# Optimization experiments

Measured on AMD Instinct MI355X. Metric: run time of the kernel, lower is better.

Reference implementation:

```python
import jax, jax.numpy as jnp
import numpy as np

B, T, C, H = 4, 2048, 1024, 16


def setup_inputs() -> dict:
    key = jax.random.key(0)
    k1, k2, k3 = jax.random.split(key, 3)
    x = jax.random.normal(k1, (B, T, C), dtype=jnp.float32)
    Wqkv = jax.random.normal(k2, (C, 3 * C), dtype=jnp.float32) * 0.02
    bqkv = jnp.zeros((3 * C,), dtype=jnp.float32)
    Wproj = jax.random.normal(k3, (C, C), dtype=jnp.float32) * 0.02
    bproj = jnp.zeros((C,), dtype=jnp.float32)
    return {"x": x, "Wqkv": Wqkv, "bqkv": bqkv, "Wproj": Wproj, "bproj": bproj}


def reference(x, Wqkv, bqkv, Wproj, bproj):
    Bx, Tx, Cx = x.shape
    head = Cx // H
    qkv = x @ Wqkv + bqkv                      # [B,T,3C]
    q, k, v = jnp.split(qkv, 3, axis=-1)
    q = q.reshape(Bx, Tx, H, head)
    k = k.reshape(Bx, Tx, H, head)
    v = v.reshape(Bx, Tx, H, head)
    scale = 1.0 / jnp.sqrt(jnp.asarray(head, dtype=x.dtype))
    scores = jnp.einsum('bqhd,bkhd->bhqk', q, k) * scale   # [B,H,T,T]
    causal = jnp.tril(jnp.ones((Tx, Tx), dtype=bool))       # [T,T]
    neg = jnp.finfo(x.dtype).min
    scores = jnp.where(causal[None, None, :, :], scores, neg)
    probs = jax.nn.softmax(scores, axis=-1)
    y = jnp.einsum('bhqk,bkhd->bqhd', probs, v).reshape(Bx, Tx, Cx)
    return y @ Wproj + bproj
```

## Files before the change

### kernel.cpp

```cpp
#include <hip/hip_runtime.h>
#include <stdint.h>

#define BB 4
#define TT 2048
#define CC 1024
#define HH 16

typedef __bf16 bf16x8 __attribute__((ext_vector_type(8)));
typedef float f32x4 __attribute__((ext_vector_type(4)));
typedef float f32x16 __attribute__((ext_vector_type(16)));
typedef unsigned short ushort8 __attribute__((ext_vector_type(8)));
typedef unsigned short ushort4v __attribute__((ext_vector_type(4)));

__device__ __forceinline__ unsigned short f2b(float f) {
    union { float f; unsigned u; } v; v.f = f;
    unsigned r = v.u + 0x7FFFu + ((v.u >> 16) & 1u);
    return (unsigned short)(r >> 16);
}
__device__ __forceinline__ unsigned pack2(float a, float b) {
    union { float f; unsigned u; } ua, ub; ua.f = a; ub.f = b;
    return __builtin_amdgcn_perm(ub.u + 0x8000u, ua.u + 0x8000u, 0x07060302u);
}
__device__ __forceinline__ float fexp2(float x) {
#if __has_builtin(__builtin_amdgcn_exp2f)
    return __builtin_amdgcn_exp2f(x);
#else
    return exp2f(x);
#endif
}
#define LOG2E 1.4426950408889634f

#define ASYNC16(gp, lp) __builtin_amdgcn_global_load_lds( \
    (const __attribute__((address_space(1))) void*)(gp),  \
    (__attribute__((address_space(3))) void*)(lp), 16, 0, 0)

__global__ __launch_bounds__(256) void k_cast(const float* __restrict__ in,
                                              unsigned short* __restrict__ out, int n) {
    int i = (blockIdx.x * 256 + threadIdx.x) * 4;
    if (i >= n) return;
    float4 v = *(const float4*)(in + i);
    ushort4v o;
    o.x = f2b(v.x); o.y = f2b(v.y); o.z = f2b(v.z); o.w = f2b(v.w);
    *(ushort4v*)(out + i) = o;
}

__global__ __launch_bounds__(256) void k_transpose_bf16(const float* __restrict__ in,
                                                        unsigned short* __restrict__ out,
                                                        int R, int Cc) {
    __shared__ float tile[32][33];
    int bx = blockIdx.x * 32, by = blockIdx.y * 32;
    int tx = threadIdx.x, ty = threadIdx.y;
    for (int i = 0; i < 32; i += 8)
        tile[ty + i][tx] = in[(size_t)(by + ty + i) * Cc + bx + tx];
    __syncthreads();
    for (int i = 0; i < 32; i += 8)
        out[(size_t)(bx + ty + i) * R + by + tx] = f2b(tile[tx][ty + i]);
}

#define QSCALE 0.125f

__global__ __launch_bounds__(256, 2) void k_gemmqkv(const unsigned short* __restrict__ A,
                                                    const unsigned short* __restrict__ Bt,
                                                    const float* __restrict__ bias,
                                                    unsigned short* __restrict__ qo,
                                                    unsigned short* __restrict__ ko,
                                                    unsigned short* __restrict__ vo,
                                                    int M, int N, int K) {
    __shared__ unsigned short sm[3 * 12288];
    const int t = threadIdx.x;
    const int lane = t & 63;
    const int c = lane & 15, qd = lane >> 4;
    const int wave = t >> 6;
    const int wr = wave >> 1, wc = wave & 1;
    const int bm = blockIdx.x * 256, bn = blockIdx.y * 128;

    f32x4 acc[8][4] = {};

    const int srow = t >> 2;
    const int sch = (t & 3) ^ ((t >> 3) & 3);
    const unsigned short* Ap = A + (size_t)(bm + srow) * K + sch * 8;
    const unsigned short* Bp = Bt + (size_t)(bn + srow) * K + sch * 8;
    const int fch = qd ^ ((c >> 1) & 3);
    const int NT = K >> 5;

#define STG_P0(buf, tt_) do {                                              \
        const unsigned short* ga_ = Ap + (size_t)(tt_) * 32;               \
        const unsigned short* gb_ = Bp + (size_t)(tt_) * 32;               \
        ASYNC16(ga_,                  &sm[(buf) * 12288 + t * 8]);         \
        ASYNC16(ga_ + (size_t)64 * K, &sm[(buf) * 12288 + 2048 + t * 8]);  \
        ASYNC16(gb_,                  &sm[(buf) * 12288 + 8192 + t * 8]);  \
    } while (0)
#define STG_P1(buf, tt_) do {                                              \
        const unsigned short* ga_ = Ap + (size_t)(tt_) * 32;               \
        const unsigned short* gb_ = Bp + (size_t)(tt_) * 32;               \
        ASYNC16(ga_ + (size_t)128 * K, &sm[(buf) * 12288 + 4096 + t * 8]); \
        ASYNC16(ga_ + (size_t)192 * K, &sm[(buf) * 12288 + 6144 + t * 8]); \
        ASYNC16(gb_ + (size_t)64 * K,  &sm[(buf) * 12288 + 10240 + t * 8]);\
    } while (0)

    STG_P0(0, 0); STG_P1(0, 0);
    STG_P0(1, 1); STG_P1(1, 1);
    asm volatile("s_waitcnt vmcnt(6)" ::: "memory");
    __builtin_amdgcn_s_barrier();

    int bc = 0, b1 = 1, bs = 2;
    for (int tt = 0; tt < NT; ++tt) {
        const unsigned short* Ab = &sm[bc * 12288];
        const unsigned short* Bb = &sm[bc * 12288 + 8192];
        bf16x8 bf_[4], af[4];

        if (tt + 2 < NT) STG_P0(bs, tt + 2);
#pragma unroll
        for (int j = 0; j < 4; j++)
            bf_[j] = *(const bf16x8*)&Bb[(wc * 64 + j * 16 + c) * 32 + fch * 8];
#pragma unroll
        for (int i = 0; i < 4; i++)
            af[i] = *(const bf16x8*)&Ab[(wr * 128 + i * 16 + c) * 32 + fch * 8];
        __builtin_amdgcn_s_barrier();
        asm volatile("s_waitcnt lgkmcnt(0)" ::: "memory");
        __builtin_amdgcn_sched_barrier(0);
        __builtin_amdgcn_s_setprio(1);
#pragma unroll
        for (int i = 0; i < 4; i++)
#pragma unroll
            for (int j = 0; j < 4; j++)
                acc[i][j] = __builtin_amdgcn_mfma_f32_16x16x32_bf16(af[i], bf_[j], acc[i][j], 0, 0, 0);
        __builtin_amdgcn_s_setprio(0);
        __builtin_amdgcn_s_barrier();

        if (tt + 2 < NT) STG_P1(bs, tt + 2);
#pragma unroll
        for (int i = 0; i < 4; i++)
            af[i] = *(const bf16x8*)&Ab[(wr * 128 + 64 + i * 16 + c) * 32 + fch * 8];
        if (tt + 2 < NT) {
            asm volatile("s_waitcnt vmcnt(6)" ::: "memory");
        } else if (tt + 1 < NT) {
            asm volatile("s_waitcnt vmcnt(0)" ::: "memory");
        }
        __builtin_amdgcn_s_barrier();
        asm volatile("s_waitcnt lgkmcnt(0)" ::: "memory");
        __builtin_amdgcn_sched_barrier(0);
        __builtin_amdgcn_s_setprio(1);
#pragma unroll
        for (int i = 0; i < 4; i++)
#pragma unroll
            for (int j = 0; j < 4; j++)
                acc[i + 4][j] = __builtin_amdgcn_mfma_f32_16x16x32_bf16(af[i], bf_[j], acc[i + 4][j], 0, 0, 0);
        __builtin_amdgcn_s_setprio(0);
        __builtin_amdgcn_s_barrier();

        int tmp = bc; bc = b1; b1 = bs; bs = tmp;
    }
#undef STG_P0
#undef STG_P1

#pragma unroll
    for (int j = 0; j < 4; j++) {
        float bv = bias[bn + wc * 64 + j * 16 + c];
#pragma unroll
        for (int i = 0; i < 8; i++)
#pragma unroll
            for (int r = 0; r < 4; r++)
                acc[i][j][r] += bv;
    }

    if (bn < 2048) {
        unsigned short* dst = (bn < 1024) ? qo : ko;
        const int dcol0 = (bn < 1024) ? bn : bn - 1024;
        const float sc = (bn < 1024) ? QSCALE : 1.0f;
        __syncthreads();
#pragma unroll
        for (int i = 0; i < 8; i++) {
            int lr0 = wr * 128 + i * 16 + qd * 4;
#pragma unroll
            for (int j = 0; j < 4; j++) {
                int col = wc * 64 + j * 16 + c;
#pragma unroll
                for (int r = 0; r < 4; r++)
                    sm[(lr0 + r) * 136 + col] = f2b(acc[i][j][r] * sc);
            }
        }
        __syncthreads();
#pragma unroll
        for (int op = 0; op < 16; op++) {
            int cid = op * 256 + t;
            int lr = cid >> 4;
            int ch = (cid & 15) * 8;
            ushort8 v = *(ushort8*)&sm[lr * 136 + ch];
            *(ushort8*)&dst[(size_t)(bm + lr) * 1024 + dcol0 + ch] = v;
        }
    } else {
        const int bseg = bm >> 11;
        const int bmt = bm & 2047;
        __syncthreads();
#pragma unroll
        for (int i = 0; i < 8; i++) {
            int tok = wr * 128 + i * 16 + qd * 4;
#pragma unroll
            for (int j = 0; j < 4; j++) {
                int dl = wc * 64 + j * 16 + c;
                ushort4v pk;
                pk.x = f2b(acc[i][j][0]); pk.y = f2b(acc[i][j][1]);
                pk.z = f2b(acc[i][j][2]); pk.w = f2b(acc[i][j][3]);
                *(ushort4v*)&sm[dl * 264 + tok] = pk;
            }
        }
        __syncthreads();
#pragma unroll
        for (int op = 0; op < 16; op++) {
            int cid = op * 256 + t;
            int dl = cid >> 5;
            int ch = (cid & 31) * 8;
            ushort8 v = *(ushort8*)&sm[dl * 264 + ch];
            int d = (bn - 2048) + dl;
            *(ushort8*)&vo[((size_t)bseg * 1024 + d) * 2048 + bmt + ch] = v;
        }
    }
}

template <int MODE>
__global__ __launch_bounds__(256) void k_gemm(const unsigned short* __restrict__ A,
                                              const unsigned short* __restrict__ Bt,
                                              const float* __restrict__ bias,
                                              float* __restrict__ outf,
                                              unsigned short* __restrict__ qo,
                                              unsigned short* __restrict__ ko,
                                              unsigned short* __restrict__ vo,
                                              int M, int N, int K) {
    __shared__ unsigned short sm[8704];
    unsigned short* As = sm;
    unsigned short* Bs = sm + 4096;
    const int t = threadIdx.x;
    const int lane = t & 63;
    const int c = lane & 15, qd = lane >> 4;
    const int wave = t >> 6;
    const int wr = (wave >> 1) * 64, wc = (wave & 1) * 64;
    const int bm = blockIdx.x * 128, bn = blockIdx.y * 128;

    f32x4 acc[4][4] = {};

    const unsigned short* Ap = A + (size_t)(bm + (t >> 2)) * K + (t & 3) * 8;
    const unsigned short* Bp = Bt + (size_t)(bn + (t >> 2)) * K + (t & 3) * 8;
    unsigned short* Asw = &As[t * 8];
    unsigned short* Bsw = &Bs[t * 8];

    for (int k0 = 0; k0 < K; k0 += 32) {
        __syncthreads();
        ASYNC16(Ap + k0, Asw);
        ASYNC16(Ap + (size_t)64 * K + k0, Asw + 2048);
        ASYNC16(Bp + k0, Bsw);
        ASYNC16(Bp + (size_t)64 * K + k0, Bsw + 2048);
        __syncthreads();
        bf16x8 af[4], bfr[4];
        for (int i = 0; i < 4; i++)
            af[i] = *(const bf16x8*)&As[(wr + i * 16 + c) * 32 + qd * 8];
        for (int j = 0; j < 4; j++)
            bfr[j] = *(const bf16x8*)&Bs[(wc + j * 16 + c) * 32 + qd * 8];
        for (int i = 0; i < 4; i++)
            for (int j = 0; j < 4; j++)
                acc[i][j] = __builtin_amdgcn_mfma_f32_16x16x32_bf16(af[i], bfr[j], acc[i][j], 0, 0, 0);
    }

    for (int j = 0; j < 4; j++) {
        float bv = bias[bn + wc + j * 16 + c];
        for (int i = 0; i < 4; i++)
            for (int r = 0; r < 4; r++)
                acc[i][j][r] += bv;
    }

    if (MODE == 0) {
        float* smf = (float*)sm;
        for (int p = 0; p < 4; p++) {
            __syncthreads();
            int lr0 = (wr >> 2) + qd * 4;
            for (int j = 0; j < 4; j++) {
                int col = wc + j * 16 + c;
                for (int r = 0; r < 4; r++)
                    smf[(lr0 + r) * 132 + col] = acc[p][j][r];
            }
            __syncthreads();
            for (int op = 0; op < 4; op++) {
                int lr = (t >> 5) + op * 8;
                int ch = (t & 31) * 4;
                float4 v = *(float4*)&smf[lr * 132 + ch];
                int grow = bm + (lr >> 4) * 64 + 16 * p + (lr & 15);
                *(float4*)&outf[(size_t)grow * N + bn + ch] = v;
            }
        }
    }
}

__global__ __launch_bounds__(256, 4) void k_attn(const unsigned short* __restrict__ q16,
                                                 const unsigned short* __restrict__ k16,
                                                 const unsigned short* __restrict__ vT16,
                                                 unsigned short* __restrict__ y16) {
    const int h = blockIdx.y, b = blockIdx.z;
    const int qi = (((int)blockIdx.x + h) & 15) ^ ((b & 1) ? 15 : 0);
    __shared__ unsigned short smem[128 * 72];
    unsigned short* q_s = smem;
    unsigned short* k_s = smem;
    unsigned short* vt_s = smem + 64 * 72;
    const int t = threadIdx.x, lane = t & 63, wave = t >> 6;
    const int l31 = lane & 31, hl = lane >> 5;
    const int wq = wave * 32;

    {
        int row = t >> 1, c32 = (t & 1) * 32;
        const unsigned short* src = q16 + ((size_t)(b * TT + qi * 128 + row)) * CC + h * 64 + c32;
        ushort8 v0 = *(const ushort8*)(src);
        ushort8 v1 = *(const ushort8*)(src + 8);
        ushort8 v2 = *(const ushort8*)(src + 16);
        ushort8 v3 = *(const ushort8*)(src + 24);
        *(ushort8*)&q_s[row * 72 + c32] = v0;
        *(ushort8*)&q_s[row * 72 + c32 + 8] = v1;
        *(ushort8*)&q_s[row * 72 + c32 + 16] = v2;
        *(ushort8*)&q_s[row * 72 + c32 + 24] = v3;
    }
    __syncthreads();
    bf16x8 qf[4];
    for (int s = 0; s < 4; s++)
        qf[s] = *(const bf16x8*)&q_s[(wq + l31) * 72 + s * 16 + hl * 8];

    f32x16 oacc[2] = {};
    float m = -3e38f, l = 0.f;
    const int qmaxw = qi * 128 + wq + 31;
    const int qminw = qi * 128 + wq;
    const int qg = qi * 128 + wq + l31;
    const int jn = 2 * qi + 2;
    const unsigned short* kbase = k16 + (size_t)b * TT * CC + h * 64;
    const unsigned short* vbase = vT16 + (((size_t)b * 16 + h) * 64) * TT;

    const int row = t >> 2, c16 = (t & 3) * 16;
    const unsigned short* ksrc = kbase + (size_t)row * CC + c16;
    const unsigned short* vsrc = vbase + (size_t)row * TT + c16;
    ushort8 ka = *(const ushort8*)ksrc, kb = *(const ushort8*)(ksrc + 8);
    ushort8 va = *(const ushort8*)vsrc, vb = *(const ushort8*)(vsrc + 8);

    for (int j = 0; j < jn; j++) {
        __syncthreads();
        *(ushort8*)&k_s[row * 72 + c16] = ka;
        *(ushort8*)&k_s[row * 72 + c16 + 8] = kb;
        *(ushort8*)&vt_s[row * 72 + c16] = va;
        *(ushort8*)&vt_s[row * 72 + c16 + 8] = vb;
        __syncthreads();
        if (j + 1 < jn) {
            const unsigned short* kn = ksrc + (size_t)(j + 1) * 64 * CC;
            const unsigned short* vn = vsrc + (j + 1) * 64;
            ka = *(const ushort8*)kn; kb = *(const ushort8*)(kn + 8);
            va = *(const ushort8*)vn; vb = *(const ushort8*)(vn + 8);
        }
        if (j * 64 > qmaxw) continue;

        f32x16 sacc[2] = {};
        for (int c2 = 0; c2 < 2; c2++)
            for (int s = 0; s < 4; s++) {
                bf16x8 kf = *(const bf16x8*)&k_s[(c2 * 32 + l31) * 72 + s * 16 + hl * 8];
                sacc[c2] = __builtin_amdgcn_mfma_f32_32x32x16_bf16(kf, qf[s], sacc[c2], 0, 0, 0);
            }

        if (j * 64 + 63 > qminw) {
            for (int c2 = 0; c2 < 2; c2++)
                for (int r = 0; r < 16; r++) {
                    int kvg = j * 64 + c2 * 32 + (r & 3) + 8 * (r >> 2) + 4 * hl;
                    if (kvg > qg) sacc[c2][r] = -1e30f;
                }
        }

        float mx = -1e30f;
        for (int c2 = 0; c2 < 2; c2++)
            for (int r = 0; r < 16; r++) mx = fmaxf(mx, sacc[c2][r]);
        mx = fmaxf(mx, __shfl_xor(mx, 32, 64));
        float mn = fmaxf(m, mx);
        float negmnl = -mn * LOG2E;
        float alpha = fexp2(fmaf(m, LOG2E, negmnl));
        m = mn;
        float sum = 0.f;
        unsigned pg[2][4][2];
        for (int c2 = 0; c2 < 2; c2++)
            for (int g = 0; g < 4; g++) {
                float p0 = fexp2(fmaf(sacc[c2][g * 4 + 0], LOG2E, negmnl));
                float p1 = fexp2(fmaf(sacc[c2][g * 4 + 1], LOG2E, negmnl));
                float p2 = fexp2(fmaf(sacc[c2][g * 4 + 2], LOG2E, negmnl));
                float p3 = fexp2(fmaf(sacc[c2][g * 4 + 3], LOG2E, negmnl));
                sum += (p0 + p1) + (p2 + p3);
                pg[c2][g][0] = pack2(p0, p1);
                pg[c2][g][1] = pack2(p2, p3);
            }
        sum += __shfl_xor(sum, 32, 64);
        l = l * alpha + sum;
        if (__ballot(alpha != 1.0f)) {
            for (int c2 = 0; c2 < 2; c2++)
                for (int r = 0; r < 16; r++) oacc[c2][r] *= alpha;
        }

        bf16x8 pf[4];
        for (int c2 = 0; c2 < 2; c2++)
            for (int pr = 0; pr < 2; pr++) {
                unsigned se0 = hl ? pg[c2][2 * pr][0] : pg[c2][2 * pr + 1][0];
                unsigned se1 = hl ? pg[c2][2 * pr][1] : pg[c2][2 * pr + 1][1];
                unsigned r0 = (unsigned)__shfl_xor((int)se0, 32, 64);
                unsigned r1 = (unsigned)__shfl_xor((int)se1, 32, 64);
                union { unsigned u[4]; bf16x8 v; } fr;
                fr.u[0] = hl ? r0 : pg[c2][2 * pr][0];
                fr.u[1] = hl ? r1 : pg[c2][2 * pr][1];
                fr.u[2] = hl ? pg[c2][2 * pr + 1][0] : r0;
                fr.u[3] = hl ? pg[c2][2 * pr + 1][1] : r1;
                pf[c2 * 2 + pr] = fr.v;
            }

        for (int s = 0; s < 4; s++)
            for (int c2o = 0; c2o < 2; c2o++) {
                bf16x8 vf = *(const bf16x8*)&vt_s[(c2o * 32 + l31) * 72 + s * 16 + hl * 8];
                oacc[c2o] = __builtin_amdgcn_mfma_f32_32x32x16_bf16(vf, pf[s], oacc[c2o], 0, 0, 0);
            }
    }

    float rl = 1.0f / l;
    size_t rowb = ((size_t)b * TT + qg) * CC + h * 64;
    for (int c2 = 0; c2 < 2; c2++)
        for (int g = 0; g < 4; g++) {
            ushort4v pk;
            pk.x = f2b(oacc[c2][g * 4 + 0] * rl);
            pk.y = f2b(oacc[c2][g * 4 + 1] * rl);
            pk.z = f2b(oacc[c2][g * 4 + 2] * rl);
            pk.w = f2b(oacc[c2][g * 4 + 3] * rl);
            *(ushort4v*)&y16[rowb + c2 * 32 + g * 8 + hl * 4] = pk;
        }
}

extern "C" void kernel_launch(void* const* d_in, const int* in_sizes, int n_in,
                              void* d_out, int out_size, void* d_ws, size_t ws_size,
                              hipStream_t stream) {
    const float* x     = (const float*)d_in[0];
    const float* Wqkv  = (const float*)d_in[1];
    const float* bqkv  = (const float*)d_in[2];
    const float* Wproj = (const float*)d_in[3];
    const float* bproj = (const float*)d_in[4];
    float* out = (float*)d_out;

    const int M = BB * TT;
    unsigned short* x16    = (unsigned short*)d_ws;
    unsigned short* y16    = x16;
    unsigned short* wqkvT  = x16 + (size_t)M * CC;
    unsigned short* wprojT = wqkvT + (size_t)3 * CC * CC;
    unsigned short* q16    = wprojT + (size_t)CC * CC;
    unsigned short* k16    = q16 + (size_t)M * CC;
    unsigned short* vT16   = k16 + (size_t)M * CC;

    k_cast<<<(M * CC) / 1024, 256, 0, stream>>>(x, x16, M * CC);
    k_transpose_bf16<<<dim3(3 * CC / 32, CC / 32), dim3(32, 8), 0, stream>>>(Wqkv, wqkvT, CC, 3 * CC);
    k_transpose_bf16<<<dim3(CC / 32, CC / 32), dim3(32, 8), 0, stream>>>(Wproj, wprojT, CC, CC);
    k_gemmqkv<<<dim3(M / 256, 3 * CC / 128), 256, 0, stream>>>(x16, wqkvT, bqkv,
                                                               q16, k16, vT16, M, 3 * CC, CC);
    k_attn<<<dim3(TT / 128, HH, BB), 256, 0, stream>>>(q16, k16, vT16, y16);
    k_gemm<0><<<dim3(M / 128, CC / 128), 256, 0, stream>>>(y16, wprojT, bproj, out,
                                                           nullptr, nullptr, nullptr, M, CC, CC);
}
```

Baseline: 257.7 us.

## Pair causal query tiles per block, lazy rescale, permlane swap, MFMA priority

```diff
diff --git a/kernel.cpp b/kernel.cpp
--- a/kernel.cpp
+++ b/kernel.cpp
@@ -295,7 +295,6 @@
                                                  const unsigned short* __restrict__ vT16,
                                                  unsigned short* __restrict__ y16) {
     const int h = blockIdx.y, b = blockIdx.z;
-    const int qi = (((int)blockIdx.x + h) & 15) ^ ((b & 1) ? 15 : 0);
     __shared__ unsigned short smem[128 * 72];
     unsigned short* q_s = smem;
     unsigned short* k_s = smem;
@@ -303,129 +302,138 @@
     const int t = threadIdx.x, lane = t & 63, wave = t >> 6;
     const int l31 = lane & 31, hl = lane >> 5;
     const int wq = wave * 32;
-
-    {
-        int row = t >> 1, c32 = (t & 1) * 32;
-        const unsigned short* src = q16 + ((size_t)(b * TT + qi * 128 + row)) * CC + h * 64 + c32;
-        ushort8 v0 = *(const ushort8*)(src);
-        ushort8 v1 = *(const ushort8*)(src + 8);
-        ushort8 v2 = *(const ushort8*)(src + 16);
-        ushort8 v3 = *(const ushort8*)(src + 24);
-        *(ushort8*)&q_s[row * 72 + c32] = v0;
-        *(ushort8*)&q_s[row * 72 + c32 + 8] = v1;
-        *(ushort8*)&q_s[row * 72 + c32 + 16] = v2;
-        *(ushort8*)&q_s[row * 72 + c32 + 24] = v3;
-    }
-    __syncthreads();
-    bf16x8 qf[4];
-    for (int s = 0; s < 4; s++)
-        qf[s] = *(const bf16x8*)&q_s[(wq + l31) * 72 + s * 16 + hl * 8];
-
-    f32x16 oacc[2] = {};
-    float m = -3e38f, l = 0.f;
-    const int qmaxw = qi * 128 + wq + 31;
-    const int qminw = qi * 128 + wq;
-    const int qg = qi * 128 + wq + l31;
-    const int jn = 2 * qi + 2;
     const unsigned short* kbase = k16 + (size_t)b * TT * CC + h * 64;
     const unsigned short* vbase = vT16 + (((size_t)b * 16 + h) * 64) * TT;
-
     const int row = t >> 2, c16 = (t & 3) * 16;
     const unsigned short* ksrc = kbase + (size_t)row * CC + c16;
     const unsigned short* vsrc = vbase + (size_t)row * TT + c16;
-    ushort8 ka = *(const ushort8*)ksrc, kb = *(const ushort8*)(ksrc + 8);
-    ushort8 va = *(const ushort8*)vsrc, vb = *(const ushort8*)(vsrc + 8);
-
-    for (int j = 0; j < jn; j++) {
-        __syncthreads();
-        *(ushort8*)&k_s[row * 72 + c16] = ka;
-        *(ushort8*)&k_s[row * 72 + c16 + 8] = kb;
-        *(ushort8*)&vt_s[row * 72 + c16] = va;
-        *(ushort8*)&vt_s[row * 72 + c16 + 8] = vb;
-        __syncthreads();
-        if (j + 1 < jn) {
-            const unsigned short* kn = ksrc + (size_t)(j + 1) * 64 * CC;
-            const unsigned short* vn = vsrc + (j + 1) * 64;
-            ka = *(const ushort8*)kn; kb = *(const ushort8*)(kn + 8);
-            va = *(const ushort8*)vn; vb = *(const ushort8*)(vn + 8);
-        }
-        if (j * 64 > qmaxw) continue;
-
-        f32x16 sacc[2] = {};
-        for (int c2 = 0; c2 < 2; c2++)
-            for (int s = 0; s < 4; s++) {
-                bf16x8 kf = *(const bf16x8*)&k_s[(c2 * 32 + l31) * 72 + s * 16 + hl * 8];
-                sacc[c2] = __builtin_amdgcn_mfma_f32_32x32x16_bf16(kf, qf[s], sacc[c2], 0, 0, 0);
-            }
-
-        if (j * 64 + 63 > qminw) {
+
+    for (int half = 0; half < 2; half++) {
+        const int qi = half ? 15 - (int)blockIdx.x : (int)blockIdx.x;
+
+        __syncthreads();
+        {
+            int qrow = t >> 1, c32 = (t & 1) * 32;
+            const unsigned short* src = q16 + ((size_t)(b * TT + qi * 128 + qrow)) * CC + h * 64 + c32;
+            ushort8 v0 = *(const ushort8*)(src);
+            ushort8 v1 = *(const ushort8*)(src + 8);
+            ushort8 v2 = *(const ushort8*)(src + 16);
+            ushort8 v3 = *(const ushort8*)(src + 24);
+            *(ushort8*)&q_s[qrow * 72 + c32] = v0;
+            *(ushort8*)&q_s[qrow * 72 + c32 + 8] = v1;
+            *(ushort8*)&q_s[qrow * 72 + c32 + 16] = v2;
+            *(ushort8*)&q_s[qrow * 72 + c32 + 24] = v3;
+        }
+        __syncthreads();
+        bf16x8 qf[4];
+        for (int s = 0; s < 4; s++)
+            qf[s] = *(const bf16x8*)&q_s[(wq + l31) * 72 + s * 16 + hl * 8];
+
+        f32x16 oacc[2] = {};
+        float m = -3e38f, l = 0.f;
+        const int qmaxw = qi * 128 + wq + 31;
+        const int qminw = qi * 128 + wq;
+        const int qg = qi * 128 + wq + l31;
+        const int jn = 2 * qi + 2;
+
+        ushort8 ka = *(const ushort8*)ksrc, kb = *(const ushort8*)(ksrc + 8);
+        ushort8 va = *(const ushort8*)vsrc, vb = *(const ushort8*)(vsrc + 8);
+
+        for (int j = 0; j < jn; j++) {
+            __syncthreads();
+            *(ushort8*)&k_s[row * 72 + c16] = ka;
+            *(ushort8*)&k_s[row * 72 + c16 + 8] = kb;
+            *(ushort8*)&vt_s[row * 72 + c16] = va;
+            *(ushort8*)&vt_s[row * 72 + c16 + 8] = vb;
+            __syncthreads();
+            if (j + 1 < jn) {
+                const unsigned short* kn = ksrc + (size_t)(j + 1) * 64 * CC;
+                const unsigned short* vn = vsrc + (j + 1) * 64;
+                ka = *(const ushort8*)kn; kb = *(const ushort8*)(kn + 8);
+                va = *(const ushort8*)vn; vb = *(const ushort8*)(vn + 8);
+            }
+            if (j * 64 > qmaxw) continue;
+
+            f32x16 sacc[2] = {};
+            __builtin_amdgcn_s_setprio(1);
             for (int c2 = 0; c2 < 2; c2++)
-                for (int r = 0; r < 16; r++) {
-                    int kvg = j * 64 + c2 * 32 + (r & 3) + 8 * (r >> 2) + 4 * hl;
-                    if (kvg > qg) sacc[c2][r] = -1e30f;
+                for (int s = 0; s < 4; s++) {
+                    bf16x8 kf = *(const bf16x8*)&k_s[(c2 * 32 + l31) * 72 + s * 16 + hl * 8];
+                    sacc[c2] = __builtin_amdgcn_mfma_f32_32x32x16_bf16(kf, qf[s], sacc[c2], 0, 0, 0);
                 }
-        }
-
-        float mx = -1e30f;
-        for (int c2 = 0; c2 < 2; c2++)
-            for (int r = 0; r < 16; r++) mx = fmaxf(mx, sacc[c2][r]);
-        mx = fmaxf(mx, __shfl_xor(mx, 32, 64));
-        float mn = fmaxf(m, mx);
-        float negmnl = -mn * LOG2E;
-        float alpha = fexp2(fmaf(m, LOG2E, negmnl));
-        m = mn;
-        float sum = 0.f;
-        unsigned pg[2][4][2];
+            __builtin_amdgcn_s_setprio(0);
+
+            if (j * 64 + 63 > qminw) {
+                for (int c2 = 0; c2 < 2; c2++)
+                    for (int r = 0; r < 16; r++) {
+                        int kvg = j * 64 + c2 * 32 + (r & 3) + 8 * (r >> 2) + 4 * hl;
+                        if (kvg > qg) sacc[c2][r] = -1e30f;
+                    }
+            }
+
+            float mx = -1e30f;
+            for (int c2 = 0; c2 < 2; c2++)
+                for (int r = 0; r < 16; r += 2)
+                    mx = fmaxf(mx, fmaxf(sacc[c2][r], sacc[c2][r + 1]));
+            mx = fmaxf(mx, __shfl_xor(mx, 32, 64));
+            if (!__all(mx <= m + 8.0f)) {
+                float mn = fmaxf(m, mx);
+                float negl = -mn * LOG2E;
+                float alpha = fexp2(fmaf(m, LOG2E, negl));
+                m = mn;
+                l *= alpha;
+                for (int c2 = 0; c2 < 2; c2++)
+                    for (int r = 0; r < 16; r++) oacc[c2][r] *= alpha;
+            }
+            float negmnl = -m * LOG2E;
+            float sum = 0.f;
+            unsigned pg[2][4][2];
+            for (int c2 = 0; c2 < 2; c2++)
+                for (int g = 0; g < 4; g++) {
+                    float p0 = fexp2(fmaf(sacc[c2][g * 4 + 0], LOG2E, negmnl));
+                    float p1 = fexp2(fmaf(sacc[c2][g * 4 + 1], LOG2E, negmnl));
+                    float p2 = fexp2(fmaf(sacc[c2][g * 4 + 2], LOG2E, negmnl));
+                    float p3 = fexp2(fmaf(sacc[c2][g * 4 + 3], LOG2E, negmnl));
+                    sum += (p0 + p1) + (p2 + p3);
+                    pg[c2][g][0] = pack2(p0, p1);
+                    pg[c2][g][1] = pack2(p2, p3);
+                }
+            sum += __shfl_xor(sum, 32, 64);
+            l += sum;
+
+            bf16x8 pf[4];
+            for (int c2 = 0; c2 < 2; c2++)
+                for (int pr = 0; pr < 2; pr++) {
+                    unsigned a0 = pg[c2][2 * pr][0], b0 = pg[c2][2 * pr + 1][0];
+                    unsigned a1 = pg[c2][2 * pr][1], b1 = pg[c2][2 * pr + 1][1];
+                    asm("v_permlane32_swap_b32 %0, %1" : "+v"(a0), "+v"(b0));
+                    asm("v_permlane32_swap_b32 %0, %1" : "+v"(a1), "+v"(b1));
+                    union { unsigned u[4]; bf16x8 v; } fr;
+                    fr.u[0] = a0; fr.u[1] = a1; fr.u[2] = b0; fr.u[3] = b1;
+                    pf[c2 * 2 + pr] = fr.v;
+                }
+
+            __builtin_amdgcn_s_setprio(1);
+            for (int s = 0; s < 4; s++)
+                for (int c2o = 0; c2o < 2; c2o++) {
+                    bf16x8 vf = *(const bf16x8*)&vt_s[(c2o * 32 + l31) * 72 + s * 16 + hl * 8];
+                    oacc[c2o] = __builtin_amdgcn_mfma_f32_32x32x16_bf16(vf, pf[s], oacc[c2o], 0, 0, 0);
+                }
+            __builtin_amdgcn_s_setprio(0);
+        }
+
+        float rl = 1.0f / l;
+        size_t rowb = ((size_t)b * TT + qg) * CC + h * 64;
         for (int c2 = 0; c2 < 2; c2++)
             for (int g = 0; g < 4; g++) {
-                float p0 = fexp2(fmaf(sacc[c2][g * 4 + 0], LOG2E, negmnl));
-                float p1 = fexp2(fmaf(sacc[c2][g * 4 + 1], LOG2E, negmnl));
-                float p2 = fexp2(fmaf(sacc[c2][g * 4 + 2], LOG2E, negmnl));
-                float p3 = fexp2(fmaf(sacc[c2][g * 4 + 3], LOG2E, negmnl));
-                sum += (p0 + p1) + (p2 + p3);
-                pg[c2][g][0] = pack2(p0, p1);
-                pg[c2][g][1] = pack2(p2, p3);
-            }
-        sum += __shfl_xor(sum, 32, 64);
-        l = l * alpha + sum;
-        if (__ballot(alpha != 1.0f)) {
-            for (int c2 = 0; c2 < 2; c2++)
-                for (int r = 0; r < 16; r++) oacc[c2][r] *= alpha;
-        }
-
-        bf16x8 pf[4];
-        for (int c2 = 0; c2 < 2; c2++)
-            for (int pr = 0; pr < 2; pr++) {
-                unsigned se0 = hl ? pg[c2][2 * pr][0] : pg[c2][2 * pr + 1][0];
-                unsigned se1 = hl ? pg[c2][2 * pr][1] : pg[c2][2 * pr + 1][1];
-                unsigned r0 = (unsigned)__shfl_xor((int)se0, 32, 64);
-                unsigned r1 = (unsigned)__shfl_xor((int)se1, 32, 64);
-                union { unsigned u[4]; bf16x8 v; } fr;
-                fr.u[0] = hl ? r0 : pg[c2][2 * pr][0];
-                fr.u[1] = hl ? r1 : pg[c2][2 * pr][1];
-                fr.u[2] = hl ? pg[c2][2 * pr + 1][0] : r0;
-                fr.u[3] = hl ? pg[c2][2 * pr + 1][1] : r1;
-                pf[c2 * 2 + pr] = fr.v;
-            }
-
-        for (int s = 0; s < 4; s++)
-            for (int c2o = 0; c2o < 2; c2o++) {
-                bf16x8 vf = *(const bf16x8*)&vt_s[(c2o * 32 + l31) * 72 + s * 16 + hl * 8];
-                oacc[c2o] = __builtin_amdgcn_mfma_f32_32x32x16_bf16(vf, pf[s], oacc[c2o], 0, 0, 0);
-            }
-    }
-
-    float rl = 1.0f / l;
-    size_t rowb = ((size_t)b * TT + qg) * CC + h * 64;
-    for (int c2 = 0; c2 < 2; c2++)
-        for (int g = 0; g < 4; g++) {
-            ushort4v pk;
-            pk.x = f2b(oacc[c2][g * 4 + 0] * rl);
-            pk.y = f2b(oacc[c2][g * 4 + 1] * rl);
-            pk.z = f2b(oacc[c2][g * 4 + 2] * rl);
-            pk.w = f2b(oacc[c2][g * 4 + 3] * rl);
-            *(ushort4v*)&y16[rowb + c2 * 32 + g * 8 + hl * 4] = pk;
-        }
+                ushort4v pk;
+                pk.x = f2b(oacc[c2][g * 4 + 0] * rl);
+                pk.y = f2b(oacc[c2][g * 4 + 1] * rl);
+                pk.z = f2b(oacc[c2][g * 4 + 2] * rl);
+                pk.w = f2b(oacc[c2][g * 4 + 3] * rl);
+                *(ushort4v*)&y16[rowb + c2 * 32 + g * 8 + hl * 4] = pk;
+            }
+    }
 }
 
 extern "C" void kernel_launch(void* const* d_in, const int* in_sizes, int n_in,
@@ -452,7 +460,7 @@
     k_transpose_bf16<<<dim3(CC / 32, CC / 32), dim3(32, 8), 0, stream>>>(Wproj, wprojT, CC, CC);
     k_gemmqkv<<<dim3(M / 256, 3 * CC / 128), 256, 0, stream>>>(x16, wqkvT, bqkv,
                                                                q16, k16, vT16, M, 3 * CC, CC);
-    k_attn<<<dim3(TT / 128, HH, BB), 256, 0, stream>>>(q16, k16, vT16, y16);
+    k_attn<<<dim3(8, HH, BB), 256, 0, stream>>>(q16, k16, vT16, y16);
     k_gemm<0><<<dim3(M / 128, CC / 128), 256, 0, stream>>>(y16, wprojT, bproj, out,
                                                            nullptr, nullptr, nullptr, M, CC, CC);
 }
```

Result: slower. 320.8 us (+24.5%).

## Triple-buffer projection GEMM with async prefetch, swizzled LDS, and split MFMA phases

Applied to the files above, without the earlier changes.

```diff
diff --git a/kernel.cpp b/kernel.cpp
--- a/kernel.cpp
+++ b/kernel.cpp
@@ -218,74 +218,121 @@
     }
 }
 
-template <int MODE>
-__global__ __launch_bounds__(256) void k_gemm(const unsigned short* __restrict__ A,
-                                              const unsigned short* __restrict__ Bt,
-                                              const float* __restrict__ bias,
-                                              float* __restrict__ outf,
-                                              unsigned short* __restrict__ qo,
-                                              unsigned short* __restrict__ ko,
-                                              unsigned short* __restrict__ vo,
-                                              int M, int N, int K) {
-    __shared__ unsigned short sm[8704];
-    unsigned short* As = sm;
-    unsigned short* Bs = sm + 4096;
+__global__ __launch_bounds__(256, 2) void k_gemmproj(const unsigned short* __restrict__ A,
+                                                     const unsigned short* __restrict__ Bt,
+                                                     const float* __restrict__ bias,
+                                                     float* __restrict__ outf,
+                                                     int M, int N, int K) {
+    __shared__ unsigned short sm[3 * 8192];
     const int t = threadIdx.x;
     const int lane = t & 63;
     const int c = lane & 15, qd = lane >> 4;
     const int wave = t >> 6;
-    const int wr = (wave >> 1) * 64, wc = (wave & 1) * 64;
+    const int wr = wave >> 1, wc = wave & 1;
     const int bm = blockIdx.x * 128, bn = blockIdx.y * 128;
 
     f32x4 acc[4][4] = {};
 
-    const unsigned short* Ap = A + (size_t)(bm + (t >> 2)) * K + (t & 3) * 8;
-    const unsigned short* Bp = Bt + (size_t)(bn + (t >> 2)) * K + (t & 3) * 8;
-    unsigned short* Asw = &As[t * 8];
-    unsigned short* Bsw = &Bs[t * 8];
-
-    for (int k0 = 0; k0 < K; k0 += 32) {
-        __syncthreads();
-        ASYNC16(Ap + k0, Asw);
-        ASYNC16(Ap + (size_t)64 * K + k0, Asw + 2048);
-        ASYNC16(Bp + k0, Bsw);
-        ASYNC16(Bp + (size_t)64 * K + k0, Bsw + 2048);
-        __syncthreads();
-        bf16x8 af[4], bfr[4];
+    const int srow = t >> 2;
+    const int sch = (t & 3) ^ ((t >> 3) & 3);
+    const unsigned short* Ap = A + (size_t)(bm + srow) * K + sch * 8;
+    const unsigned short* Bp = Bt + (size_t)(bn + srow) * K + sch * 8;
+    const int fch = qd ^ ((c >> 1) & 3);
+    const int NT = K >> 5;
+
+#define PSTG_A(buf, tt_) do {                                              \
+        const unsigned short* ga_ = Ap + (size_t)(tt_) * 32;               \
+        ASYNC16(ga_,                  &sm[(buf) * 8192 + t * 8]);          \
+        ASYNC16(ga_ + (size_t)64 * K, &sm[(buf) * 8192 + 2048 + t * 8]);   \
+    } while (0)
+#define PSTG_B(buf, tt_) do {                                              \
+        const unsigned short* gb_ = Bp + (size_t)(tt_) * 32;               \
+        ASYNC16(gb_,                  &sm[(buf) * 8192 + 4096 + t * 8]);   \
+        ASYNC16(gb_ + (size_t)64 * K, &sm[(buf) * 8192 + 6144 + t * 8]);   \
+    } while (0)
+
+    PSTG_A(0, 0); PSTG_B(0, 0);
+    PSTG_A(1, 1); PSTG_B(1, 1);
+    asm volatile("s_waitcnt vmcnt(4)" ::: "memory");
+    __builtin_amdgcn_s_barrier();
+
+    int bc = 0, b1 = 1, bs = 2;
+    for (int tt = 0; tt < NT; ++tt) {
+        const unsigned short* Ab = &sm[bc * 8192];
+        const unsigned short* Bb = &sm[bc * 8192 + 4096];
+        bf16x8 bf_[4], af[2];
+
+        if (tt + 2 < NT) PSTG_A(bs, tt + 2);
+#pragma unroll
+        for (int j = 0; j < 4; j++)
+            bf_[j] = *(const bf16x8*)&Bb[(wc * 64 + j * 16 + c) * 32 + fch * 8];
+#pragma unroll
+        for (int i = 0; i < 2; i++)
+            af[i] = *(const bf16x8*)&Ab[(wr * 64 + i * 16 + c) * 32 + fch * 8];
+        __builtin_amdgcn_s_barrier();
+        asm volatile("s_waitcnt lgkmcnt(0)" ::: "memory");
+        __builtin_amdgcn_sched_barrier(0);
+        __builtin_amdgcn_s_setprio(1);
+#pragma unroll
+        for (int i = 0; i < 2; i++)
+#pragma unroll
+            for (int j = 0; j < 4; j++)
+                acc[i][j] = __builtin_amdgcn_mfma_f32_16x16x32_bf16(af[i], bf_[j], acc[i][j], 0, 0, 0);
+        __builtin_amdgcn_s_setprio(0);
+        __builtin_amdgcn_s_barrier();
+
+        if (tt + 2 < NT) PSTG_B(bs, tt + 2);
+#pragma unroll
+        for (int i = 0; i < 2; i++)
+            af[i] = *(const bf16x8*)&Ab[(wr * 64 + 32 + i * 16 + c) * 32 + fch * 8];
+        if (tt + 2 < NT) {
+            asm volatile("s_waitcnt vmcnt(4)" ::: "memory");
+        } else if (tt + 1 < NT) {
+            asm volatile("s_waitcnt vmcnt(0)" ::: "memory");
+        }
+        __builtin_amdgcn_s_barrier();
+        asm volatile("s_waitcnt lgkmcnt(0)" ::: "memory");
+        __builtin_amdgcn_sched_barrier(0);
+        __builtin_amdgcn_s_setprio(1);
+#pragma unroll
+        for (int i = 0; i < 2; i++)
+#pragma unroll
+            for (int j = 0; j < 4; j++)
+                acc[i + 2][j] = __builtin_amdgcn_mfma_f32_16x16x32_bf16(af[i], bf_[j], acc[i + 2][j], 0, 0, 0);
+        __builtin_amdgcn_s_setprio(0);
+        __builtin_amdgcn_s_barrier();
+
+        int tmp = bc; bc = b1; b1 = bs; bs = tmp;
+    }
+#undef PSTG_A
+#undef PSTG_B
+
+#pragma unroll
+    for (int j = 0; j < 4; j++) {
+        float bv = bias[bn + wc * 64 + j * 16 + c];
+#pragma unroll
         for (int i = 0; i < 4; i++)
-            af[i] = *(const bf16x8*)&As[(wr + i * 16 + c) * 32 + qd * 8];
-        for (int j = 0; j < 4; j++)
-            bfr[j] = *(const bf16x8*)&Bs[(wc + j * 16 + c) * 32 + qd * 8];
-        for (int i = 0; i < 4; i++)
-            for (int j = 0; j < 4; j++)
-                acc[i][j] = __builtin_amdgcn_mfma_f32_16x16x32_bf16(af[i], bfr[j], acc[i][j], 0, 0, 0);
-    }
-
-    for (int j = 0; j < 4; j++) {
-        float bv = bias[bn + wc + j * 16 + c];
-        for (int i = 0; i < 4; i++)
+#pragma unroll
             for (int r = 0; r < 4; r++)
                 acc[i][j][r] += bv;
     }
 
-    if (MODE == 0) {
-        float* smf = (float*)sm;
-        for (int p = 0; p < 4; p++) {
-            __syncthreads();
-            int lr0 = (wr >> 2) + qd * 4;
-            for (int j = 0; j < 4; j++) {
-                int col = wc + j * 16 + c;
-                for (int r = 0; r < 4; r++)
-                    smf[(lr0 + r) * 132 + col] = acc[p][j][r];
-            }
-            __syncthreads();
-            for (int op = 0; op < 4; op++) {
-                int lr = (t >> 5) + op * 8;
-                int ch = (t & 31) * 4;
-                float4 v = *(float4*)&smf[lr * 132 + ch];
-                int grow = bm + (lr >> 4) * 64 + 16 * p + (lr & 15);
-                *(float4*)&outf[(size_t)grow * N + bn + ch] = v;
-            }
+    float* smf = (float*)sm;
+    for (int p = 0; p < 4; p++) {
+        __syncthreads();
+        int lr0 = wr * 16 + qd * 4;
+        for (int j = 0; j < 4; j++) {
+            int col = wc * 64 + j * 16 + c;
+            for (int r = 0; r < 4; r++)
+                smf[(lr0 + r) * 132 + col] = acc[p][j][r];
+        }
+        __syncthreads();
+        for (int op = 0; op < 4; op++) {
+            int lr = (t >> 5) + op * 8;
+            int ch = (t & 31) * 4;
+            float4 v = *(float4*)&smf[lr * 132 + ch];
+            int grow = bm + (lr >> 4) * 64 + 16 * p + (lr & 15);
+            *(float4*)&outf[(size_t)grow * N + bn + ch] = v;
         }
     }
 }
@@ -453,6 +500,5 @@
     k_gemmqkv<<<dim3(M / 256, 3 * CC / 128), 256, 0, stream>>>(x16, wqkvT, bqkv,
                                                                q16, k16, vT16, M, 3 * CC, CC);
     k_attn<<<dim3(TT / 128, HH, BB), 256, 0, stream>>>(q16, k16, vT16, y16);
-    k_gemm<0><<<dim3(M / 128, CC / 128), 256, 0, stream>>>(y16, wprojT, bproj, out,
-                                                           nullptr, nullptr, nullptr, M, CC, CC);
-}
+    k_gemmproj<<<dim3(M / 128, CC / 128), 256, 0, stream>>>(y16, wprojT, bproj, out, M, CC, CC);
+}
```

New measurement: 247.9 us. 3.8% less time.
